# Optimization experiments

Hardware: AMD Instinct MI355X
Metric: run time of the kernel (lower is better)

The kernel has to match this reference:

```python
import jax, jax.numpy as jnp
import numpy as np

N, E, D = 50000, 512000, 128

def mish(x):
    return x * jnp.tanh(jax.nn.softplus(x))

def ln(x, g, b):
    m = jnp.mean(x, axis=-1, keepdims=True)
    v = jnp.var(x, axis=-1, keepdims=True)
    return (x - m) / jnp.sqrt(v + 1e-5) * g + b

def setup_inputs():
    key = jax.random.key(0)
    ks = jax.random.split(key, 16)
    W = lambda k, i, o: jax.random.normal(k, (i, o), jnp.float32) * 0.02
    z = jnp.zeros((D,), jnp.float32)
    o = jnp.ones((D,), jnp.float32)
    return {
        "node_feat": jax.random.normal(ks[0], (N, D), jnp.float32),
        "coord_feat": jax.random.normal(ks[1], (N, D), jnp.float32),
        "Wq": W(ks[2], D, D), "bq": z, "gq": o, "beq": z,
        "Wk": W(ks[3], D, D), "bk": z, "gk": o, "bek": z,
        "Wm1": W(ks[4], D, D), "bm1": z, "gm": o, "bem": z,
        "Wm2": W(ks[5], D, D), "bm2": z,
        "Wb1": W(ks[6], D, D), "bb1": z, "gb": o, "beb": z,
        "Wb2": W(ks[7], D, D), "bb2": z,
        "Ww1": W(ks[8], D, D), "bw1": z, "gw": o, "bew": z,
        "Ww2": W(ks[9], D, D), "bw2": z,
        "Wn1": W(ks[10], 2 * D, D), "bn1": z,
        "Wn2": W(ks[11], D, D), "bn2": z,
        "Wc1": W(ks[12], D, D), "bc1": z,
        "Wc2": W(ks[13], D, D),
        "src": jax.random.randint(ks[14], (E,), 0, N, jnp.int32),
        "dst": jax.random.randint(ks[15], (E,), 0, N, jnp.int32),
    }

def reference(node_feat, coord_feat, Wq, bq, gq, beq, Wk, bk, gk, bek,
              Wm1, bm1, gm, bem, Wm2, bm2, Wb1, bb1, gb, beb, Wb2, bb2,
              Ww1, bw1, gw, bew, Ww2, bw2, Wn1, bn1, Wn2, bn2, Wc1, bc1, Wc2,
              src, dst):
    # linear_q / linear_k on coord features: Linear -> LayerNorm -> Mish
    q = mish(ln(coord_feat @ Wq + bq, gq, beq))   # [N, D]
    k = mish(ln(coord_feat @ Wk + bk, gk, bek))   # [N, D]
    # u_sub_v('q','k'): per-edge q[src] - k[dst]
    rel = q[src] - k[dst]                          # [E, D]
    radial = jnp.sum(rel * rel, axis=-1, keepdims=True)  # [E, 1]
    rel = rel / jnp.sqrt(radial + 1e-8)
    # relative position encodings from dst coord features
    xd = coord_feat[dst]                           # [E, D]
    pem = mish(ln(xd @ Wm1 + bm1, gm, bem)) @ Wm2 + bm2
    peb = mish(ln(xd @ Wb1 + bb1, gb, beb)) @ Wb2 + bb2
    rel = rel * pem + peb
    # weight_encoding MLP
    w = mish(ln(rel @ Ww1 + bw1, gw, bew)) @ Ww2 + bw2  # [E, D]
    # dgl.softmax_edges over a single graph: softmax across the edge axis
    w = jax.nn.softmax(w, axis=0)
    # update_all(copy_e, sum): scatter-add edge weights to destination nodes
    h_neigh = jax.ops.segment_sum(w, dst, num_segments=N)  # [N, D]
    h = mish(jnp.concatenate([node_feat, h_neigh], axis=-1) @ Wn1 + bn1) @ Wn2 + bn2
    x = mish(coord_feat @ Wc1 + bc1) @ Wc2
    return (h, x)
```

## Files before the change

kernel.cpp:

```cpp
#include <hip/hip_runtime.h>
#include <cstdint>
#include <cstddef>

#define DN 128
#define NND 50000
#define NED 512000
#define NSCAN 49

typedef __attribute__((ext_vector_type(8))) short bf8;
typedef __attribute__((ext_vector_type(4))) float f4;
typedef unsigned short us;

__device__ __forceinline__ us f2bf(float f){
  union { float f; unsigned int u; } c; c.f = f;
  unsigned int r = c.u + 0x7fffu + ((c.u >> 16) & 1u);
  return (us)(r >> 16);
}
__device__ __forceinline__ float bf2f(us u){
  union { unsigned int u; float f; } c; c.u = ((unsigned int)u) << 16;
  return c.f;
}
__device__ __forceinline__ float mishf(float x){
  float e = __expf(x);
  float u = 1.f + e;
  float u2 = u * u;
  float t = (u2 - 1.f) / (u2 + 1.f);
  return x * ((x > 20.f) ? 1.f : t);
}

#define MFMA16(a, b, c) __builtin_amdgcn_mfma_f32_16x16x32_bf16((a), (b), (c), 0, 0, 0)

__device__ __forceinline__ bf8 lds_frag(const us* base, int row, int rowStrideB, int kElem){
  int byte = row * rowStrideB + kElem * 2;
  byte ^= (row & 7) << 4;
  return *(const bf8*)((const char*)base + byte);
}
__device__ __forceinline__ bf8 gfrag(const us* W, int n, int K, int kElem){
  return *(const bf8*)(W + (size_t)n * K + kElem);
}

template<int OUT_BF16>
__device__ __forceinline__ void store_tile(void* outp, int nrows, int r0,
                                           int wr, int wc, int g, int s, int ostride,
                                           const f4 (&A)[2][4]){
#pragma unroll
  for (int rt = 0; rt < 2; ++rt)
#pragma unroll
    for (int ct = 0; ct < 4; ++ct)
#pragma unroll
      for (int reg = 0; reg < 4; ++reg){
        int row = r0 + wr*32 + rt*16 + g*4 + reg;
        if (row < nrows){
          int col = wc*64 + ct*16 + s;
          float v = A[rt][ct][reg];
          if constexpr (OUT_BF16 != 0)
            ((us*)outp)[(size_t)row*ostride + col] = f2bf(v);
          else
            ((float*)outp)[(size_t)row*ostride + col] = v;
        }
      }
}

__device__ __forceinline__ void gemm_reg(const bf8 (&a)[2][4], const us* __restrict__ WT,
                                         const float* __restrict__ bias,
                                         int wc, int g, int s, f4 (&acc)[2][4]){
#pragma unroll
  for (int ct = 0; ct < 4; ++ct){
    float bv = bias ? bias[wc*64 + ct*16 + s] : 0.f;
    f4 t = {bv, bv, bv, bv};
    acc[0][ct] = t; acc[1][ct] = t;
  }
#pragma unroll
  for (int ct = 0; ct < 4; ++ct){
    int n = wc*64 + ct*16 + s;
#pragma unroll
    for (int kk = 0; kk < 4; ++kk){
      bf8 b = gfrag(WT, n, DN, kk*32 + g*8);
      acc[0][ct] = MFMA16(a[0][kk], b, acc[0][ct]);
      acc[1][ct] = MFMA16(a[1][kk], b, acc[1][ct]);
    }
  }
}

__device__ __forceinline__ void ln_mish(f4 (&acc)[2][4],
                                        const float* __restrict__ gam,
                                        const float* __restrict__ bet,
                                        int wr, int wc, int g, int s,
                                        float (*rowsum)[64][2], float (*rowsq)[64][2],
                                        int buf){
  float gv[4], bev[4];
#pragma unroll
  for (int ct = 0; ct < 4; ++ct){ int n = wc*64 + ct*16 + s; gv[ct] = gam[n]; bev[ct] = bet[n]; }
#pragma unroll
  for (int rt = 0; rt < 2; ++rt)
#pragma unroll
    for (int reg = 0; reg < 4; ++reg){
      float sm = acc[rt][0][reg] + acc[rt][1][reg] + acc[rt][2][reg] + acc[rt][3][reg];
      float sq = acc[rt][0][reg]*acc[rt][0][reg] + acc[rt][1][reg]*acc[rt][1][reg]
               + acc[rt][2][reg]*acc[rt][2][reg] + acc[rt][3][reg]*acc[rt][3][reg];
#pragma unroll
      for (int m = 1; m < 16; m <<= 1){ sm += __shfl_xor(sm, m, 64); sq += __shfl_xor(sq, m, 64); }
      if (s == 0){
        int row = wr*32 + rt*16 + g*4 + reg;
        rowsum[buf][row][wc] = sm; rowsq[buf][row][wc] = sq;
      }
    }
  __syncthreads();
#pragma unroll
  for (int rt = 0; rt < 2; ++rt)
#pragma unroll
    for (int reg = 0; reg < 4; ++reg){
      int row = wr*32 + rt*16 + g*4 + reg;
      float sm = rowsum[buf][row][0] + rowsum[buf][row][1];
      float sq = rowsq[buf][row][0] + rowsq[buf][row][1];
      float mu = sm * (1.f/128.f);
      float var = sq * (1.f/128.f) - mu*mu;
      float rs = rsqrtf(var + 1e-5f);
#pragma unroll
      for (int ct = 0; ct < 4; ++ct)
        acc[rt][ct][reg] = mishf((acc[rt][ct][reg] - mu) * rs * gv[ct] + bev[ct]);
    }
}

__device__ __forceinline__ void write_T(us* Tsh, int wr, int wc, int g, int s,
                                        const f4 (&A)[2][4]){
#pragma unroll
  for (int rt = 0; rt < 2; ++rt)
#pragma unroll
    for (int ct = 0; ct < 4; ++ct)
#pragma unroll
      for (int reg = 0; reg < 4; ++reg){
        int row = wr*32 + rt*16 + g*4 + reg;
        int col = wc*64 + ct*16 + s;
        int byte = row*256 + col*2; byte ^= (row & 7) << 4;
        *(us*)((char*)Tsh + byte) = f2bf(A[rt][ct][reg]);
      }
}

__device__ __forceinline__ void load_a2(const us* Tsh, int wr, int g, int s, bf8 (&a2)[2][4]){
#pragma unroll
  for (int rt = 0; rt < 2; ++rt)
#pragma unroll
    for (int kk = 0; kk < 4; ++kk)
      a2[rt][kk] = lds_frag(Tsh, wr*32 + rt*16 + s, 256, kk*32 + g*8);
}

__global__ __launch_bounds__(256, 2)
void node_fused(const float* __restrict__ X,
                const us* __restrict__ WqT,  const float* __restrict__ bq,
                const float* __restrict__ gq, const float* __restrict__ beq,
                const us* __restrict__ WkT,  const float* __restrict__ bk,
                const float* __restrict__ gk, const float* __restrict__ bek,
                const us* __restrict__ Wm1T, const float* __restrict__ bm1,
                const float* __restrict__ gm, const float* __restrict__ bem,
                const us* __restrict__ Wm2T, const float* __restrict__ bm2,
                const us* __restrict__ Wb1T, const float* __restrict__ bb1,
                const float* __restrict__ gb, const float* __restrict__ beb,
                const us* __restrict__ Wb2T, const float* __restrict__ bb2,
                const us* __restrict__ Wc1T, const float* __restrict__ bc1,
                const us* __restrict__ Wc2T,
                us* __restrict__ qt, us* __restrict__ kmb, float* __restrict__ xout)
{
  __shared__ us Ash[64 * DN];
  __shared__ float rowsum[2][64][2];
  __shared__ float rowsq[2][64][2];

  const int tid = threadIdx.x;
  const int r0 = blockIdx.x * 64;

  {
    int r = tid >> 2, c4 = tid & 3;
    int grow = r0 + r; if (grow >= NND) grow = NND - 1;
    const f4* sp = (const f4*)(X + (size_t)grow * DN + c4 * 32);
#pragma unroll
    for (int j = 0; j < 4; ++j){
      f4 v0 = sp[2*j], v1 = sp[2*j+1];
      bf8 o;
#pragma unroll
      for (int q = 0; q < 4; ++q){ o[q] = (short)f2bf(v0[q]); o[4+q] = (short)f2bf(v1[q]); }
      int byte = r*256 + c4*64 + j*16; byte ^= (r & 7) << 4;
      *(bf8*)((char*)Ash + byte) = o;
    }
  }
  __syncthreads();

  const int lane = tid & 63, w = tid >> 6;
  const int wr = w >> 1, wc = w & 1;
  const int g = lane >> 4, s = lane & 15;

  bf8 a[2][4];
#pragma unroll
  for (int rt = 0; rt < 2; ++rt)
#pragma unroll
    for (int kk = 0; kk < 4; ++kk)
      a[rt][kk] = lds_frag(Ash, wr*32 + rt*16 + s, 256, kk*32 + g*8);
  __syncthreads();

  f4 acc[2][4], acc2[2][4];
  bf8 a2[2][4];

  gemm_reg(a, WqT, bq, wc, g, s, acc);
  ln_mish(acc, gq, beq, wr, wc, g, s, rowsum, rowsq, 0);
  store_tile<1>((void*)qt, NND, r0, wr, wc, g, s, DN, acc);

  gemm_reg(a, WkT, bk, wc, g, s, acc);
  ln_mish(acc, gk, bek, wr, wc, g, s, rowsum, rowsq, 1);
  store_tile<1>((void*)kmb, NND, r0, wr, wc, g, s, 384, acc);

  gemm_reg(a, Wm1T, bm1, wc, g, s, acc);
  ln_mish(acc, gm, bem, wr, wc, g, s, rowsum, rowsq, 0);
  write_T(Ash, wr, wc, g, s, acc);
  __syncthreads();
  load_a2(Ash, wr, g, s, a2);
#pragma unroll
  for (int ct = 0; ct < 4; ++ct){
    float bv = bm2[wc*64 + ct*16 + s]; f4 t = {bv,bv,bv,bv}; acc2[0][ct] = t; acc2[1][ct] = t;
  }
#pragma unroll
  for (int ct = 0; ct < 4; ++ct){
    int n = wc*64 + ct*16 + s;
#pragma unroll
    for (int kk = 0; kk < 4; ++kk){
      bf8 b = gfrag(Wm2T, n, DN, kk*32 + g*8);
      acc2[0][ct] = MFMA16(a2[0][kk], b, acc2[0][ct]);
      acc2[1][ct] = MFMA16(a2[1][kk], b, acc2[1][ct]);
    }
  }
  store_tile<1>((void*)(kmb + 128), NND, r0, wr, wc, g, s, 384, acc2);

  gemm_reg(a, Wb1T, bb1, wc, g, s, acc);
  ln_mish(acc, gb, beb, wr, wc, g, s, rowsum, rowsq, 1);
  write_T(Ash, wr, wc, g, s, acc);
  __syncthreads();
  load_a2(Ash, wr, g, s, a2);
#pragma unroll
  for (int ct = 0; ct < 4; ++ct){
    float bv = bb2[wc*64 + ct*16 + s]; f4 t = {bv,bv,bv,bv}; acc2[0][ct] = t; acc2[1][ct] = t;
  }
#pragma unroll
  for (int ct = 0; ct < 4; ++ct){
    int n = wc*64 + ct*16 + s;
#pragma unroll
    for (int kk = 0; kk < 4; ++kk){
      bf8 b = gfrag(Wb2T, n, DN, kk*32 + g*8);
      acc2[0][ct] = MFMA16(a2[0][kk], b, acc2[0][ct]);
      acc2[1][ct] = MFMA16(a2[1][kk], b, acc2[1][ct]);
    }
  }
  store_tile<1>((void*)(kmb + 256), NND, r0, wr, wc, g, s, 384, acc2);

  gemm_reg(a, Wc1T, bc1, wc, g, s, acc);
#pragma unroll
  for (int rt = 0; rt < 2; ++rt)
#pragma unroll
    for (int ct = 0; ct < 4; ++ct)
#pragma unroll
      for (int reg = 0; reg < 4; ++reg)
        acc[rt][ct][reg] = mishf(acc[rt][ct][reg]);
  __syncthreads();
  write_T(Ash, wr, wc, g, s, acc);
  __syncthreads();
  load_a2(Ash, wr, g, s, a2);
#pragma unroll
  for (int ct = 0; ct < 4; ++ct){ f4 t = {0,0,0,0}; acc2[0][ct] = t; acc2[1][ct] = t; }
#pragma unroll
  for (int ct = 0; ct < 4; ++ct){
    int n = wc*64 + ct*16 + s;
#pragma unroll
    for (int kk = 0; kk < 4; ++kk){
      bf8 b = gfrag(Wc2T, n, DN, kk*32 + g*8);
      acc2[0][ct] = MFMA16(a2[0][kk], b, acc2[0][ct]);
      acc2[1][ct] = MFMA16(a2[1][kk], b, acc2[1][ct]);
    }
  }
  store_tile<0>((void*)xout, NND, r0, wr, wc, g, s, DN, acc2);
}

__global__ void csr_count(const int* __restrict__ dst, int* __restrict__ deg){
  int e = blockIdx.x * 256 + threadIdx.x;
  if (e < NED) atomicAdd(&deg[dst[e]], 1);
}

__global__ __launch_bounds__(1024) void csr_blocksum(const int* __restrict__ deg,
                                                     int* __restrict__ bsum){
  __shared__ int sb[1024];
  int t = threadIdx.x, idx = blockIdx.x * 1024 + t;
  sb[t] = (idx < NND) ? deg[idx] : 0;
  __syncthreads();
  for (int off = 512; off > 0; off >>= 1){
    if (t < off) sb[t] += sb[t + off];
    __syncthreads();
  }
  if (t == 0) bsum[blockIdx.x] = sb[0];
}

__global__ void csr_scanroot(const int* __restrict__ bsum, int* __restrict__ boff){
  if (threadIdx.x == 0){
    int run = 0;
    for (int b = 0; b < NSCAN; ++b){ boff[b] = run; run += bsum[b]; }
  }
}

__global__ __launch_bounds__(1024) void csr_scatter(const int* __restrict__ deg,
                                                    const int* __restrict__ boff,
                                                    int* __restrict__ fillctr){
  __shared__ int ss[1024];
  int t = threadIdx.x, idx = blockIdx.x * 1024 + t;
  int v = (idx < NND) ? deg[idx] : 0;
  ss[t] = v;
  __syncthreads();
  for (int off = 1; off < 1024; off <<= 1){
    int x = (t >= off) ? ss[t - off] : 0;
    __syncthreads();
    ss[t] += x;
    __syncthreads();
  }
  if (idx < NND){
    int p = boff[blockIdx.x] + ss[t] - v;
    fillctr[idx] = p;
  }
}

__global__ void csr_fill(const int* __restrict__ src, const int* __restrict__ dst,
                         int* __restrict__ fillctr,
                         int* __restrict__ ssorted, int* __restrict__ dsorted){
  int e = blockIdx.x * 256 + threadIdx.x;
  if (e < NED){
    int d = dst[e];
    int p = atomicAdd(&fillctr[d], 1);
    ssorted[p] = src[e];
    dsorted[p] = d;
  }
}

__global__ __launch_bounds__(256, 2)
void edge_kernel(const us* __restrict__ qtab,
                 const us* __restrict__ kmb,
                 const us* __restrict__ W1T,
                 const us* __restrict__ W2T,
                 const float* __restrict__ bw1,
                 const float* __restrict__ gwp,
                 const float* __restrict__ bewp,
                 const float* __restrict__ bw2,
                 const int* __restrict__ ssorted,
                 const int* __restrict__ dsorted,
                 float* __restrict__ hacc,
                 float* __restrict__ colsum8)
{
  __shared__ us Ash[64 * DN];
  __shared__ float rowsum[1][64][2];
  __shared__ float rowsq[1][64][2];
  __shared__ int dsh[64];

  const int tid = threadIdx.x;
  const int nchunk = gridDim.x >> 3;
  const int swz = (blockIdx.x & 7) * nchunk + (blockIdx.x >> 3);
  const int e0 = swz * 64;
  const int lane = tid & 63, w = tid >> 6;
  const int wr = w >> 1, wc = w & 1;
  const int g = lane >> 4, s = lane & 15;

  if (tid < 64) dsh[tid] = dsorted[e0 + tid];

  bf8 B1[4][4], B2[4][4];
  float b1v[4], gv[4], bev[4], b2v[4];
#pragma unroll
  for (int ct = 0; ct < 4; ++ct){
    int n = wc*64 + ct*16 + s;
#pragma unroll
    for (int kk = 0; kk < 4; ++kk){
      B1[ct][kk] = gfrag(W1T, n, DN, kk*32 + g*8);
      B2[ct][kk] = gfrag(W2T, n, DN, kk*32 + g*8);
    }
    b1v[ct] = bw1[n]; gv[ct] = gwp[n]; bev[ct] = bewp[n]; b2v[ct] = bw2[n];
  }

  {
    int r = tid >> 2, c4 = tid & 3;
    int e = e0 + r;
    int sn = ssorted[e], dn = dsorted[e];
    const bf8* qp = (const bf8*)(qtab + (size_t)sn * DN + c4 * 32);
    const us* kb = kmb + (size_t)dn * 384 + c4 * 32;
    float rel[32]; float ss = 0.f;
#pragma unroll
    for (int j = 0; j < 4; ++j){
      bf8 qv = qp[j];
      bf8 kv = *(const bf8*)(kb + j*8);
#pragma unroll
      for (int q = 0; q < 8; ++q){
        float d = bf2f((us)qv[q]) - bf2f((us)kv[q]);
        rel[j*8+q] = d; ss += d * d;
      }
    }
    ss += __shfl_xor(ss, 1, 64);
    ss += __shfl_xor(ss, 2, 64);
    float rinv = rsqrtf(ss + 1e-8f);
#pragma unroll
    for (int j = 0; j < 4; ++j){
      bf8 mv = *(const bf8*)(kb + 128 + j*8);
      bf8 bv = *(const bf8*)(kb + 256 + j*8);
      bf8 o;
#pragma unroll
      for (int q = 0; q < 8; ++q){
        float v = rel[j*8+q] * rinv * bf2f((us)mv[q]) + bf2f((us)bv[q]);
        o[q] = (short)f2bf(v);
      }
      int byte = r*256 + c4*64 + j*16; byte ^= (r & 7) << 4;
      *(bf8*)((char*)Ash + byte) = o;
    }
  }
  __syncthreads();

  f4 acc[2][4];
#pragma unroll
  for (int ct = 0; ct < 4; ++ct){ f4 t = {b1v[ct], b1v[ct], b1v[ct], b1v[ct]}; acc[0][ct] = t; acc[1][ct] = t; }
  bf8 a[2][4];
#pragma unroll
  for (int rt = 0; rt < 2; ++rt)
#pragma unroll
    for (int kk = 0; kk < 4; ++kk)
      a[rt][kk] = lds_frag(Ash, wr*32 + rt*16 + s, 256, kk*32 + g*8);
#pragma unroll
  for (int ct = 0; ct < 4; ++ct)
#pragma unroll
    for (int kk = 0; kk < 4; ++kk){
      acc[0][ct] = MFMA16(a[0][kk], B1[ct][kk], acc[0][ct]);
      acc[1][ct] = MFMA16(a[1][kk], B1[ct][kk], acc[1][ct]);
    }

#pragma unroll
  for (int rt = 0; rt < 2; ++rt)
#pragma unroll
    for (int reg = 0; reg < 4; ++reg){
      float sm = acc[rt][0][reg] + acc[rt][1][reg] + acc[rt][2][reg] + acc[rt][3][reg];
      float sq = acc[rt][0][reg]*acc[rt][0][reg] + acc[rt][1][reg]*acc[rt][1][reg]
               + acc[rt][2][reg]*acc[rt][2][reg] + acc[rt][3][reg]*acc[rt][3][reg];
#pragma unroll
      for (int m = 1; m < 16; m <<= 1){ sm += __shfl_xor(sm, m, 64); sq += __shfl_xor(sq, m, 64); }
      if (s == 0){
        int row = wr*32 + rt*16 + g*4 + reg;
        rowsum[0][row][wc] = sm; rowsq[0][row][wc] = sq;
      }
    }
  __syncthreads();
#pragma unroll
  for (int rt = 0; rt < 2; ++rt)
#pragma unroll
    for (int reg = 0; reg < 4; ++reg){
      int row = wr*32 + rt*16 + g*4 + reg;
      float sm = rowsum[0][row][0] + rowsum[0][row][1];
      float sq = rowsq[0][row][0] + rowsq[0][row][1];
      float mu = sm * (1.f/128.f);
      float var = sq * (1.f/128.f) - mu*mu;
      float rs = rsqrtf(var + 1e-5f);
#pragma unroll
      for (int ct = 0; ct < 4; ++ct)
        acc[rt][ct][reg] = mishf((acc[rt][ct][reg] - mu) * rs * gv[ct] + bev[ct]);
    }

  write_T(Ash, wr, wc, g, s, acc);
  __syncthreads();

  f4 p[2][4];
#pragma unroll
  for (int ct = 0; ct < 4; ++ct){ f4 t = {b2v[ct], b2v[ct], b2v[ct], b2v[ct]}; p[0][ct] = t; p[1][ct] = t; }
  bf8 a2[2][4];
  load_a2(Ash, wr, g, s, a2);
#pragma unroll
  for (int ct = 0; ct < 4; ++ct)
#pragma unroll
    for (int kk = 0; kk < 4; ++kk){
      p[0][ct] = MFMA16(a2[0][kk], B2[ct][kk], p[0][ct]);
      p[1][ct] = MFMA16(a2[1][kk], B2[ct][kk], p[1][ct]);
    }
#pragma unroll
  for (int rt = 0; rt < 2; ++rt)
#pragma unroll
    for (int ct = 0; ct < 4; ++ct)
#pragma unroll
      for (int reg = 0; reg < 4; ++reg)
        p[rt][ct][reg] = __expf(p[rt][ct][reg]);

  __syncthreads();

  write_T(Ash, wr, wc, g, s, p);
  __syncthreads();

  {
    int col = tid & 127, half = tid >> 7;
    int rbeg = half * 32;
    float csum = 0.f;
    int prev = dsh[rbeg];
    float run = 0.f;
#pragma unroll 8
    for (int r = rbeg; r < rbeg + 32; ++r){
      int d = dsh[r];
      int byte = r*256 + col*2; byte ^= (r & 7) << 4;
      float v = bf2f(*(const us*)((const char*)Ash + byte));
      csum += v;
      if (d != prev){
        atomicAdd(&hacc[(size_t)prev * DN + col], run);
        run = v; prev = d;
      } else {
        run += v;
      }
    }
    atomicAdd(&hacc[(size_t)prev * DN + col], run);
    atomicAdd(&colsum8[(blockIdx.x & 7) * DN + col], csum);
  }
}

__global__ __launch_bounds__(256, 2)
void final_h(const float* __restrict__ nodef,
             const float* __restrict__ hacc,
             const float* __restrict__ colsum8,
             const us* __restrict__ Wn1T,
             const float* __restrict__ bn1,
             const us* __restrict__ Wn2T,
             const float* __restrict__ bn2,
             float* __restrict__ outh)
{
  __shared__ us Ash[64 * 256];
  __shared__ float rcs[DN];

  const int tid = threadIdx.x;
  const int r0 = blockIdx.x * 64;

  if (tid < DN){
    float ssum = 0.f;
#pragma unroll
    for (int x = 0; x < 8; ++x) ssum += colsum8[x * DN + tid];
    rcs[tid] = 1.f / ssum;
  }
  __syncthreads();

  {
    int r = tid >> 2, c4 = tid & 3;
    int grow = r0 + r; if (grow >= NND) grow = NND - 1;
    const f4* np = (const f4*)(nodef + (size_t)grow * DN + c4 * 32);
    const f4* hp = (const f4*)(hacc + (size_t)grow * DN + c4 * 32);
#pragma unroll
    for (int j = 0; j < 4; ++j){
      f4 v0 = np[2*j], v1 = np[2*j+1];
      bf8 o;
#pragma unroll
      for (int q = 0; q < 4; ++q){ o[q] = (short)f2bf(v0[q]); o[4+q] = (short)f2bf(v1[q]); }
      int byte = r*512 + c4*64 + j*16; byte ^= (r & 7) << 4;
      *(bf8*)((char*)Ash + byte) = o;
      f4 h0 = hp[2*j], h1 = hp[2*j+1];
      bf8 o2;
#pragma unroll
      for (int q = 0; q < 4; ++q){
        o2[q]   = (short)f2bf(h0[q] * rcs[c4*32 + j*8 + q]);
        o2[4+q] = (short)f2bf(h1[q] * rcs[c4*32 + j*8 + 4 + q]);
      }
      int byte2 = r*512 + 256 + c4*64 + j*16; byte2 ^= (r & 7) << 4;
      *(bf8*)((char*)Ash + byte2) = o2;
    }
  }
  __syncthreads();

  const int lane = tid & 63, w = tid >> 6;
  const int wr = w >> 1, wc = w & 1;
  const int g = lane >> 4, s = lane & 15;

  float b1v[4], b2v[4];
#pragma unroll
  for (int ct = 0; ct < 4; ++ct){ int n = wc*64 + ct*16 + s; b1v[ct] = bn1[n]; b2v[ct] = bn2[n]; }

  f4 acc[2][4];
#pragma unroll
  for (int ct = 0; ct < 4; ++ct){ f4 t = {b1v[ct], b1v[ct], b1v[ct], b1v[ct]}; acc[0][ct] = t; acc[1][ct] = t; }

  bf8 a[2][8];
#pragma unroll
  for (int rt = 0; rt < 2; ++rt)
#pragma unroll
    for (int kk = 0; kk < 8; ++kk)
      a[rt][kk] = lds_frag(Ash, wr*32 + rt*16 + s, 512, kk*32 + g*8);
  __syncthreads();

#pragma unroll
  for (int ct = 0; ct < 4; ++ct){
    int n = wc*64 + ct*16 + s;
#pragma unroll
    for (int kk = 0; kk < 8; ++kk){
      bf8 b = gfrag(Wn1T, n, 256, kk*32 + g*8);
      acc[0][ct] = MFMA16(a[0][kk], b, acc[0][ct]);
      acc[1][ct] = MFMA16(a[1][kk], b, acc[1][ct]);
    }
  }

#pragma unroll
  for (int rt = 0; rt < 2; ++rt)
#pragma unroll
    for (int ct = 0; ct < 4; ++ct)
#pragma unroll
      for (int reg = 0; reg < 4; ++reg)
        acc[rt][ct][reg] = mishf(acc[rt][ct][reg]);
  write_T((us*)Ash, wr, wc, g, s, acc);
  __syncthreads();

  f4 acc2[2][4];
#pragma unroll
  for (int ct = 0; ct < 4; ++ct){ f4 t = {b2v[ct], b2v[ct], b2v[ct], b2v[ct]}; acc2[0][ct] = t; acc2[1][ct] = t; }
  bf8 a2[2][4];
  load_a2((const us*)Ash, wr, g, s, a2);
#pragma unroll
  for (int ct = 0; ct < 4; ++ct){
    int n = wc*64 + ct*16 + s;
#pragma unroll
    for (int kk = 0; kk < 4; ++kk){
      bf8 b = gfrag(Wn2T, n, DN, kk*32 + g*8);
      acc2[0][ct] = MFMA16(a2[0][kk], b, acc2[0][ct]);
      acc2[1][ct] = MFMA16(a2[1][kk], b, acc2[1][ct]);
    }
  }
  store_tile<0>((void*)outh, NND, r0, wr, wc, g, s, DN, acc2);
}

struct WPrepArgs {
  const float* w[12];
  us* wt[12];
  int K[12];
};

__global__ void prep_weights(WPrepArgs a){
  int widx = blockIdx.y;
  int K = a.K[widx];
  int idx = blockIdx.x * 256 + threadIdx.x;
  if (idx >= DN * K) return;
  int kshift = (K == 256) ? 8 : 7;
  int n = idx >> kshift;
  int k = idx & (K - 1);
  a.wt[widx][idx] = f2bf(a.w[widx][(size_t)k * DN + n]);
}

extern "C" void kernel_launch(void* const* d_in, const int* in_sizes, int n_in,
                              void* d_out, int out_size, void* d_ws, size_t ws_size,
                              hipStream_t stream) {
  const float* node_feat = (const float*)d_in[0];
  const float* coordf    = (const float*)d_in[1];
  const float* Wq  = (const float*)d_in[2];
  const float* bq  = (const float*)d_in[3];
  const float* gq  = (const float*)d_in[4];
  const float* beq = (const float*)d_in[5];
  const float* Wk  = (const float*)d_in[6];
  const float* bk  = (const float*)d_in[7];
  const float* gk  = (const float*)d_in[8];
  const float* bek = (const float*)d_in[9];
  const float* Wm1 = (const float*)d_in[10];
  const float* bm1 = (const float*)d_in[11];
  const float* gm  = (const float*)d_in[12];
  const float* bem = (const float*)d_in[13];
  const float* Wm2 = (const float*)d_in[14];
  const float* bm2 = (const float*)d_in[15];
  const float* Wb1 = (const float*)d_in[16];
  const float* bb1 = (const float*)d_in[17];
  const float* gb  = (const float*)d_in[18];
  const float* beb = (const float*)d_in[19];
  const float* Wb2 = (const float*)d_in[20];
  const float* bb2 = (const float*)d_in[21];
  const float* Ww1 = (const float*)d_in[22];
  const float* bw1 = (const float*)d_in[23];
  const float* gw  = (const float*)d_in[24];
  const float* bew = (const float*)d_in[25];
  const float* Ww2 = (const float*)d_in[26];
  const float* bw2 = (const float*)d_in[27];
  const float* Wn1 = (const float*)d_in[28];
  const float* bn1 = (const float*)d_in[29];
  const float* Wn2 = (const float*)d_in[30];
  const float* bn2 = (const float*)d_in[31];
  const float* Wc1 = (const float*)d_in[32];
  const float* bc1 = (const float*)d_in[33];
  const float* Wc2 = (const float*)d_in[34];
  const int* srcI  = (const int*)d_in[35];
  const int* dstI  = (const int*)d_in[36];

  char* ws = (char*)d_ws;
  size_t off = 0;
  auto alloc = [&](size_t bytes) -> char* {
    char* p = ws + off;
    off += (bytes + 255) & ~(size_t)255;
    return p;
  };
  us*    qt      = (us*)alloc((size_t)NND * DN * 2);
  us*    kmb     = (us*)alloc((size_t)NND * 384 * 2);
  float* hacc    = (float*)alloc((size_t)NND * DN * 4);
  float* colsum8 = (float*)alloc(8 * DN * 4);
  int*   deg     = (int*)alloc((size_t)NND * 4);
  int*   fillctr = (int*)alloc((size_t)NND * 4);
  int*   ssorted = (int*)alloc((size_t)NED * 4);
  int*   dsorted = (int*)alloc((size_t)NED * 4);
  int*   bsum    = (int*)alloc((size_t)NSCAN * 4);
  int*   boff    = (int*)alloc((size_t)NSCAN * 4);
  us*    wtb     = (us*)alloc((size_t)12 * 16384 * 2);

  hipMemsetAsync(hacc, 0, (size_t)NND * DN * 4 + 8 * DN * 4, stream);
  hipMemsetAsync(deg, 0, (size_t)NND * 4, stream);

  WPrepArgs pa;
  const float* wsrc[12] = {Wq, Wk, Wm1, Wm2, Wb1, Wb2, Ww1, Ww2, Wc1, Wc2, Wn2, Wn1};
  for (int i = 0; i < 12; ++i){
    pa.w[i] = wsrc[i];
    pa.wt[i] = wtb + (size_t)i * 16384;
    pa.K[i] = (i == 11) ? 256 : 128;
  }
  prep_weights<<<dim3(128, 12), 256, 0, stream>>>(pa);

  csr_count<<<(NED + 255) / 256, 256, 0, stream>>>(dstI, deg);
  csr_blocksum<<<NSCAN, 1024, 0, stream>>>(deg, bsum);
  csr_scanroot<<<1, 64, 0, stream>>>(bsum, boff);
  csr_scatter<<<NSCAN, 1024, 0, stream>>>(deg, boff, fillctr);
  csr_fill<<<(NED + 255) / 256, 256, 0, stream>>>(srcI, dstI, fillctr, ssorted, dsorted);

  const int NB = (NND + 63) / 64;

  node_fused<<<NB, 256, 0, stream>>>(coordf,
      pa.wt[0], bq, gq, beq,
      pa.wt[1], bk, gk, bek,
      pa.wt[2], bm1, gm, bem, pa.wt[3], bm2,
      pa.wt[4], bb1, gb, beb, pa.wt[5], bb2,
      pa.wt[8], bc1, pa.wt[9],
      qt, kmb, (float*)d_out + (size_t)NND * DN);

  edge_kernel<<<NED / 64, 256, 0, stream>>>(qt, kmb, pa.wt[6], pa.wt[7],
                                            bw1, gw, bew, bw2, ssorted, dsorted,
                                            hacc, colsum8);

  final_h<<<NB, 256, 0, stream>>>(node_feat, hacc, colsum8,
                                  pa.wt[11], bn1, pa.wt[10], bn2, (float*)d_out);
}
```

Baseline: 517.1 us.

## Make edge kernel persistent with software-prefetched gathers across edge tiles

The edge kernel now launches a fixed grid of 512 blocks. Each block loops over a contiguous range of 64-edge tiles and prefetches the next tile's q/k/m/b gathers and indices into registers while the current tile runs its two MFMA stages. A second LDS buffer separates the gathered rel tile from the MLP intermediates, and the dst indices are double-buffered. Weight fragments are no longer held in registers; they are reloaded from global memory (likely L1/L2-resident) on every tile. This trades register pressure and fewer block launches against repeated weight loads and possibly lower occupancy.

```diff
diff --git a/kernel.cpp b/kernel.cpp
--- a/kernel.cpp
+++ b/kernel.cpp
@@ -5,6 +5,8 @@
 #define DN 128
 #define NND 50000
 #define NED 512000
+#define NTILES 8000
+#define EGRID 512
 #define NSCAN 49
 
 typedef __attribute__((ext_vector_type(8))) short bf8;
@@ -348,165 +350,201 @@
                  float* __restrict__ colsum8)
 {
   __shared__ us Ash[64 * DN];
+  __shared__ us Tsh[64 * DN];
   __shared__ float rowsum[1][64][2];
   __shared__ float rowsq[1][64][2];
-  __shared__ int dsh[64];
+  __shared__ int dsh[2][64];
 
   const int tid = threadIdx.x;
-  const int nchunk = gridDim.x >> 3;
-  const int swz = (blockIdx.x & 7) * nchunk + (blockIdx.x >> 3);
-  const int e0 = swz * 64;
   const int lane = tid & 63, w = tid >> 6;
   const int wr = w >> 1, wc = w & 1;
   const int g = lane >> 4, s = lane & 15;
-
-  if (tid < 64) dsh[tid] = dsorted[e0 + tid];
-
-  bf8 B1[4][4], B2[4][4];
+  const int r = tid >> 2, c4 = tid & 3;
+
+  const int swz = (blockIdx.x & 7) * (EGRID >> 3) + (blockIdx.x >> 3);
+  const int beg = (int)(((long long)swz * NTILES) / EGRID);
+  const int end = (int)(((long long)(swz + 1) * NTILES) / EGRID);
+
   float b1v[4], gv[4], bev[4], b2v[4];
 #pragma unroll
   for (int ct = 0; ct < 4; ++ct){
     int n = wc*64 + ct*16 + s;
-#pragma unroll
-    for (int kk = 0; kk < 4; ++kk){
-      B1[ct][kk] = gfrag(W1T, n, DN, kk*32 + g*8);
-      B2[ct][kk] = gfrag(W2T, n, DN, kk*32 + g*8);
-    }
     b1v[ct] = bw1[n]; gv[ct] = gwp[n]; bev[ct] = bewp[n]; b2v[ct] = bw2[n];
   }
 
+  int dc = dsorted[beg*64 + r];
+  bf8 qv[4], kv[4], mv[4], bv[4];
   {
-    int r = tid >> 2, c4 = tid & 3;
-    int e = e0 + r;
-    int sn = ssorted[e], dn = dsorted[e];
-    const bf8* qp = (const bf8*)(qtab + (size_t)sn * DN + c4 * 32);
-    const us* kb = kmb + (size_t)dn * 384 + c4 * 32;
-    float rel[32]; float ss = 0.f;
+    int sn0 = ssorted[beg*64 + r];
+    const bf8* qp = (const bf8*)(qtab + (size_t)sn0 * DN + c4 * 32);
+    const us*  kb = kmb + (size_t)dc * 384 + c4 * 32;
 #pragma unroll
     for (int j = 0; j < 4; ++j){
-      bf8 qv = qp[j];
-      bf8 kv = *(const bf8*)(kb + j*8);
-#pragma unroll
-      for (int q = 0; q < 8; ++q){
-        float d = bf2f((us)qv[q]) - bf2f((us)kv[q]);
-        rel[j*8+q] = d; ss += d * d;
-      }
-    }
-    ss += __shfl_xor(ss, 1, 64);
-    ss += __shfl_xor(ss, 2, 64);
-    float rinv = rsqrtf(ss + 1e-8f);
-#pragma unroll
-    for (int j = 0; j < 4; ++j){
-      bf8 mv = *(const bf8*)(kb + 128 + j*8);
-      bf8 bv = *(const bf8*)(kb + 256 + j*8);
-      bf8 o;
-#pragma unroll
-      for (int q = 0; q < 8; ++q){
-        float v = rel[j*8+q] * rinv * bf2f((us)mv[q]) + bf2f((us)bv[q]);
-        o[q] = (short)f2bf(v);
-      }
-      int byte = r*256 + c4*64 + j*16; byte ^= (r & 7) << 4;
-      *(bf8*)((char*)Ash + byte) = o;
-    }
-  }
-  __syncthreads();
-
-  f4 acc[2][4];
-#pragma unroll
-  for (int ct = 0; ct < 4; ++ct){ f4 t = {b1v[ct], b1v[ct], b1v[ct], b1v[ct]}; acc[0][ct] = t; acc[1][ct] = t; }
-  bf8 a[2][4];
-#pragma unroll
-  for (int rt = 0; rt < 2; ++rt)
-#pragma unroll
-    for (int kk = 0; kk < 4; ++kk)
-      a[rt][kk] = lds_frag(Ash, wr*32 + rt*16 + s, 256, kk*32 + g*8);
-#pragma unroll
-  for (int ct = 0; ct < 4; ++ct)
-#pragma unroll
-    for (int kk = 0; kk < 4; ++kk){
-      acc[0][ct] = MFMA16(a[0][kk], B1[ct][kk], acc[0][ct]);
-      acc[1][ct] = MFMA16(a[1][kk], B1[ct][kk], acc[1][ct]);
-    }
-
-#pragma unroll
-  for (int rt = 0; rt < 2; ++rt)
-#pragma unroll
-    for (int reg = 0; reg < 4; ++reg){
-      float sm = acc[rt][0][reg] + acc[rt][1][reg] + acc[rt][2][reg] + acc[rt][3][reg];
-      float sq = acc[rt][0][reg]*acc[rt][0][reg] + acc[rt][1][reg]*acc[rt][1][reg]
-               + acc[rt][2][reg]*acc[rt][2][reg] + acc[rt][3][reg]*acc[rt][3][reg];
-#pragma unroll
-      for (int m = 1; m < 16; m <<= 1){ sm += __shfl_xor(sm, m, 64); sq += __shfl_xor(sq, m, 64); }
-      if (s == 0){
+      qv[j] = qp[j];
+      kv[j] = *(const bf8*)(kb + j*8);
+      mv[j] = *(const bf8*)(kb + 128 + j*8);
+      bv[j] = *(const bf8*)(kb + 256 + j*8);
+    }
+  }
+  int snN = 0, dnN = 0, dcN = dc;
+  if (beg + 1 < end){
+    snN = ssorted[(beg+1)*64 + r];
+    dnN = dsorted[(beg+1)*64 + r];
+  }
+
+  for (int t = beg; t < end; ++t){
+    const int par = t & 1;
+
+    {
+      float rel[32]; float ss = 0.f;
+#pragma unroll
+      for (int j = 0; j < 4; ++j){
+#pragma unroll
+        for (int q = 0; q < 8; ++q){
+          float d = bf2f((us)qv[j][q]) - bf2f((us)kv[j][q]);
+          rel[j*8+q] = d; ss += d * d;
+        }
+      }
+      ss += __shfl_xor(ss, 1, 64);
+      ss += __shfl_xor(ss, 2, 64);
+      float rinv = rsqrtf(ss + 1e-8f);
+#pragma unroll
+      for (int j = 0; j < 4; ++j){
+        bf8 o;
+#pragma unroll
+        for (int q = 0; q < 8; ++q){
+          float v = rel[j*8+q] * rinv * bf2f((us)mv[j][q]) + bf2f((us)bv[j][q]);
+          o[q] = (short)f2bf(v);
+        }
+        int byte = r*256 + c4*64 + j*16; byte ^= (r & 7) << 4;
+        *(bf8*)((char*)Ash + byte) = o;
+      }
+    }
+    if (c4 == 0) dsh[par][r] = dc;
+
+    if (t + 1 < end){
+      const bf8* qp = (const bf8*)(qtab + (size_t)snN * DN + c4 * 32);
+      const us*  kb = kmb + (size_t)dnN * 384 + c4 * 32;
+#pragma unroll
+      for (int j = 0; j < 4; ++j){
+        qv[j] = qp[j];
+        kv[j] = *(const bf8*)(kb + j*8);
+        mv[j] = *(const bf8*)(kb + 128 + j*8);
+        bv[j] = *(const bf8*)(kb + 256 + j*8);
+      }
+      dcN = dnN;
+      if (t + 2 < end){
+        snN = ssorted[(t+2)*64 + r];
+        dnN = dsorted[(t+2)*64 + r];
+      }
+    }
+    __syncthreads();
+
+    f4 acc[2][4];
+#pragma unroll
+    for (int ct = 0; ct < 4; ++ct){ f4 tt = {b1v[ct], b1v[ct], b1v[ct], b1v[ct]}; acc[0][ct] = tt; acc[1][ct] = tt; }
+    bf8 a[2][4];
+#pragma unroll
+    for (int rt = 0; rt < 2; ++rt)
+#pragma unroll
+      for (int kk = 0; kk < 4; ++kk)
+        a[rt][kk] = lds_frag(Ash, wr*32 + rt*16 + s, 256, kk*32 + g*8);
+#pragma unroll
+    for (int ct = 0; ct < 4; ++ct){
+      int n = wc*64 + ct*16 + s;
+#pragma unroll
+      for (int kk = 0; kk < 4; ++kk){
+        bf8 b = gfrag(W1T, n, DN, kk*32 + g*8);
+        acc[0][ct] = MFMA16(a[0][kk], b, acc[0][ct]);
+        acc[1][ct] = MFMA16(a[1][kk], b, acc[1][ct]);
+      }
+    }
+
+#pragma unroll
+    for (int rt = 0; rt < 2; ++rt)
+#pragma unroll
+      for (int reg = 0; reg < 4; ++reg){
+        float sm = acc[rt][0][reg] + acc[rt][1][reg] + acc[rt][2][reg] + acc[rt][3][reg];
+        float sq = acc[rt][0][reg]*acc[rt][0][reg] + acc[rt][1][reg]*acc[rt][1][reg]
+                 + acc[rt][2][reg]*acc[rt][2][reg] + acc[rt][3][reg]*acc[rt][3][reg];
+#pragma unroll
+        for (int m = 1; m < 16; m <<= 1){ sm += __shfl_xor(sm, m, 64); sq += __shfl_xor(sq, m, 64); }
+        if (s == 0){
+          int row = wr*32 + rt*16 + g*4 + reg;
+          rowsum[0][row][wc] = sm; rowsq[0][row][wc] = sq;
+        }
+      }
+    __syncthreads();
+
+#pragma unroll
+    for (int rt = 0; rt < 2; ++rt)
+#pragma unroll
+      for (int reg = 0; reg < 4; ++reg){
         int row = wr*32 + rt*16 + g*4 + reg;
-        rowsum[0][row][wc] = sm; rowsq[0][row][wc] = sq;
-      }
-    }
-  __syncthreads();
-#pragma unroll
-  for (int rt = 0; rt < 2; ++rt)
-#pragma unroll
-    for (int reg = 0; reg < 4; ++reg){
-      int row = wr*32 + rt*16 + g*4 + reg;
-      float sm = rowsum[0][row][0] + rowsum[0][row][1];
-      float sq = rowsq[0][row][0] + rowsq[0][row][1];
-      float mu = sm * (1.f/128.f);
-      float var = sq * (1.f/128.f) - mu*mu;
-      float rs = rsqrtf(var + 1e-5f);
+        float sm = rowsum[0][row][0] + rowsum[0][row][1];
+        float sq = rowsq[0][row][0] + rowsq[0][row][1];
+        float mu = sm * (1.f/128.f);
+        float var = sq * (1.f/128.f) - mu*mu;
+        float rs = rsqrtf(var + 1e-5f);
+#pragma unroll
+        for (int ct = 0; ct < 4; ++ct)
+          acc[rt][ct][reg] = mishf((acc[rt][ct][reg] - mu) * rs * gv[ct] + bev[ct]);
+      }
+
+    write_T(Tsh, wr, wc, g, s, acc);
+    __syncthreads();
+
+    f4 p[2][4];
+#pragma unroll
+    for (int ct = 0; ct < 4; ++ct){ f4 tt = {b2v[ct], b2v[ct], b2v[ct], b2v[ct]}; p[0][ct] = tt; p[1][ct] = tt; }
+    bf8 a2[2][4];
+    load_a2(Tsh, wr, g, s, a2);
+#pragma unroll
+    for (int ct = 0; ct < 4; ++ct){
+      int n = wc*64 + ct*16 + s;
+#pragma unroll
+      for (int kk = 0; kk < 4; ++kk){
+        bf8 b = gfrag(W2T, n, DN, kk*32 + g*8);
+        p[0][ct] = MFMA16(a2[0][kk], b, p[0][ct]);
+        p[1][ct] = MFMA16(a2[1][kk], b, p[1][ct]);
+      }
+    }
+#pragma unroll
+    for (int rt = 0; rt < 2; ++rt)
 #pragma unroll
       for (int ct = 0; ct < 4; ++ct)
-        acc[rt][ct][reg] = mishf((acc[rt][ct][reg] - mu) * rs * gv[ct] + bev[ct]);
-    }
-
-  write_T(Ash, wr, wc, g, s, acc);
-  __syncthreads();
-
-  f4 p[2][4];
-#pragma unroll
-  for (int ct = 0; ct < 4; ++ct){ f4 t = {b2v[ct], b2v[ct], b2v[ct], b2v[ct]}; p[0][ct] = t; p[1][ct] = t; }
-  bf8 a2[2][4];
-  load_a2(Ash, wr, g, s, a2);
-#pragma unroll
-  for (int ct = 0; ct < 4; ++ct)
-#pragma unroll
-    for (int kk = 0; kk < 4; ++kk){
-      p[0][ct] = MFMA16(a2[0][kk], B2[ct][kk], p[0][ct]);
-      p[1][ct] = MFMA16(a2[1][kk], B2[ct][kk], p[1][ct]);
-    }
-#pragma unroll
-  for (int rt = 0; rt < 2; ++rt)
-#pragma unroll
-    for (int ct = 0; ct < 4; ++ct)
-#pragma unroll
-      for (int reg = 0; reg < 4; ++reg)
-        p[rt][ct][reg] = __expf(p[rt][ct][reg]);
-
-  __syncthreads();
-
-  write_T(Ash, wr, wc, g, s, p);
-  __syncthreads();
-
-  {
-    int col = tid & 127, half = tid >> 7;
-    int rbeg = half * 32;
-    float csum = 0.f;
-    int prev = dsh[rbeg];
-    float run = 0.f;
+#pragma unroll
+        for (int reg = 0; reg < 4; ++reg)
+          p[rt][ct][reg] = __expf(p[rt][ct][reg]);
+    __syncthreads();
+
+    write_T(Tsh, wr, wc, g, s, p);
+    __syncthreads();
+
+    {
+      int col = tid & 127, half = tid >> 7;
+      int rbeg = half * 32;
+      float csum = 0.f;
+      int prev = dsh[par][rbeg];
+      float run = 0.f;
 #pragma unroll 8
-    for (int r = rbeg; r < rbeg + 32; ++r){
-      int d = dsh[r];
-      int byte = r*256 + col*2; byte ^= (r & 7) << 4;
-      float v = bf2f(*(const us*)((const char*)Ash + byte));
-      csum += v;
-      if (d != prev){
-        atomicAdd(&hacc[(size_t)prev * DN + col], run);
-        run = v; prev = d;
-      } else {
-        run += v;
-      }
-    }
-    atomicAdd(&hacc[(size_t)prev * DN + col], run);
-    atomicAdd(&colsum8[(blockIdx.x & 7) * DN + col], csum);
+      for (int r2 = rbeg; r2 < rbeg + 32; ++r2){
+        int d = dsh[par][r2];
+        int byte = r2*256 + col*2; byte ^= (r2 & 7) << 4;
+        float v = bf2f(*(const us*)((const char*)Tsh + byte));
+        csum += v;
+        if (d != prev){
+          atomicAdd(&hacc[(size_t)prev * DN + col], run);
+          run = v; prev = d;
+        } else {
+          run += v;
+        }
+      }
+      atomicAdd(&hacc[(size_t)prev * DN + col], run);
+      atomicAdd(&colsum8[(blockIdx.x & 7) * DN + col], csum);
+    }
+
+    dc = dcN;
   }
 }
 
@@ -724,9 +762,9 @@
       pa.wt[8], bc1, pa.wt[9],
       qt, kmb, (float*)d_out + (size_t)NND * DN);
 
-  edge_kernel<<<NED / 64, 256, 0, stream>>>(qt, kmb, pa.wt[6], pa.wt[7],
-                                            bw1, gw, bew, bw2, ssorted, dsorted,
-                                            hacc, colsum8);
+  edge_kernel<<<EGRID, 256, 0, stream>>>(qt, kmb, pa.wt[6], pa.wt[7],
+                                         bw1, gw, bew, bw2, ssorted, dsorted,
+                                         hacc, colsum8);
 
   final_h<<<NB, 256, 0, stream>>>(node_feat, hacc, colsum8,
                                   pa.wt[11], bn1, pa.wt[10], bn2, (float*)d_out);
```

New measurement: 640.9 us. 23.9% more time.
